# Kernel tuning notes

Measured on AMD Instinct MI355X. Metric: run time of the kernel, lower is better.

## Reference

```python
import jax, jax.numpy as jnp
from jax import lax
import numpy as np

H, W = 240, 304
IN_CH, OUT_CH, K = 16, 32, 3
B = 8
N_PER = 65536
N = B * N_PER
CIN = IN_CH + 2  # pos + neg + features


def setup_inputs() -> dict:
    key = jax.random.key(0)
    k1, k2, k3, k4, k5 = jax.random.split(key, 5)
    # events columns: x, y, t in [0,1); polarity in {0,1}
    xyt = jax.random.uniform(k1, (N, 3), dtype=jnp.float32)
    pol = jax.random.randint(k2, (N, 1), 0, 2).astype(jnp.float32)
    events = jnp.concatenate([xyt, pol], axis=1)
    features = jax.random.normal(k3, (N, IN_CH), dtype=jnp.float32)
    offsets = (jnp.arange(1, B + 1, dtype=jnp.int64) * N_PER)  # cumulative counts
    # SubmanifoldConvolution params: one [CIN, OUT_CH] matrix per filter offset -> HWIO
    fan_in = K * K * CIN
    weight = jax.random.normal(k4, (K, K, CIN, OUT_CH), dtype=jnp.float32) / np.sqrt(fan_in)
    bias = jax.random.normal(k5, (OUT_CH,), dtype=jnp.float32) * 0.01
    return {"events": events, "features": features, "weight": weight,
            "bias": bias, "offsets": offsets}


def reference(events, features, weight, bias, offsets):
    n = events.shape[0]
    b = offsets.shape[0]
    # offset2batch: row i belongs to first sample whose cumulative offset exceeds i
    batch = jnp.searchsorted(offsets, jnp.arange(n, dtype=offsets.dtype), side="right").astype(jnp.int32)
    pos = events[:, 3:4]
    neg = 1.0 - pos
    sparse = jnp.concatenate([pos, neg, features], axis=1)  # [N, CIN]
    # yx = events[:, [1, 0]] scaled by (h, w), rounded to grid coords
    yi = jnp.clip(jnp.round(events[:, 1] * H).astype(jnp.int32), 0, H - 1)
    xi = jnp.clip(jnp.round(events[:, 0] * W).astype(jnp.int32), 0, W - 1)
    key = (batch * H + yi) * W + xi  # linear site id, [N]
    nseg = b * H * W
    # scn InputLayer mode=4: average features of duplicate coordinates
    feat_sum = jax.ops.segment_sum(sparse, key, num_segments=nseg)  # [nseg, CIN]
    cnt = jax.ops.segment_sum(jnp.ones((n,), sparse.dtype), key, num_segments=nseg)
    dense = feat_sum / jnp.maximum(cnt, 1.0)[:, None]
    dense = dense.reshape(b, H, W, CIN)  # zeros at inactive sites
    # Submanifold 3x3 conv: inactive neighbors are zero, so a dense SAME conv
    # evaluated only at active sites matches the submanifold rulebook math.
    out = lax.conv_general_dilated(dense, weight, window_strides=(1, 1),
                                   padding="SAME",
                                   dimension_numbers=("NHWC", "HWIO", "NHWC"))
    out = out.reshape(nseg, OUT_CH)
    # OutputLayer: read back per input row (active sites only), add bias there
    f = out[key] + bias  # [N, OUT_CH]
    return f
```

## Files before the change

kernel.cpp:

```cpp
#include <hip/hip_runtime.h>

#define Hh 240
#define Ww 304
#define IN_CH 16
#define OUT_CH 32
#define Bb 8
#define N_PER 65536
#define N_EV (Bb * N_PER)
#define CIN (IN_CH + 2)
#define NSEG (Bb * Hh * Ww)
#define NBLK 570

#define DP 10

#define TW 32
#define TH 8
#define HW_ 34
#define HH_ 10
#define NXT_TILES 10
#define NYT_TILES 30
#define OPITCH 33
#define HALO_DW (HH_ * HW_ * DP)
#define HALO_LD 3424

typedef __attribute__((ext_vector_type(8))) short bf16x8;
typedef __attribute__((ext_vector_type(4))) float f32x4;

__device__ __forceinline__ unsigned short f2bf(float x) {
  unsigned u = __float_as_uint(x);
  unsigned r = u + 0x7fffu + ((u >> 16) & 1u);
  return (unsigned short)(r >> 16);
}
__device__ __forceinline__ float bf2f(unsigned short b) {
  return __uint_as_float(((unsigned)b) << 16);
}
__device__ __forceinline__ unsigned pk2(float a, float b) {
  return (unsigned)f2bf(a) | ((unsigned)f2bf(b) << 16);
}

__global__ __launch_bounds__(256) void hist_rank_kernel(
    const float* __restrict__ events, const int* __restrict__ offsets,
    int* __restrict__ hist, int2* __restrict__ kr) {
  int i = blockIdx.x * blockDim.x + threadIdx.x;
  float4 ev = ((const float4*)events)[i];
  int yi = (int)rintf(ev.y * (float)Hh);
  yi = min(max(yi, 0), Hh - 1);
  int xi = (int)rintf(ev.x * (float)Ww);
  xi = min(max(xi, 0), Ww - 1);
  int b = 0;
#pragma unroll
  for (int j = 0; j < Bb; j++) b += (offsets[j] <= i) ? 1 : 0;
  int key = (b * Hh + yi) * Ww + xi;
  int pol = (ev.w != 0.0f) ? 1 : 0;
  int rank = atomicAdd(&hist[key], 1);
  kr[i] = make_int2(key | (pol << 31), rank);
}

__global__ __launch_bounds__(256) void scan1_kernel(int* __restrict__ data,
                                                    int* __restrict__ blockSum) {
  __shared__ int lds[256];
  int b = blockIdx.x, t = threadIdx.x;
  int idx = b * 1024 + t * 4;
  int4 v = *(const int4*)(data + idx);
  int s0 = v.x, s1 = s0 + v.y, s2 = s1 + v.z, s3 = s2 + v.w;
  lds[t] = s3;
  __syncthreads();
  int val = s3;
  for (int off = 1; off < 256; off <<= 1) {
    int n = (t >= off) ? lds[t - off] : 0;
    __syncthreads();
    val += n;
    lds[t] = val;
    __syncthreads();
  }
  int excl = val - s3;
  int4 o;
  o.x = excl; o.y = excl + s0; o.z = excl + s1; o.w = excl + s2;
  *(int4*)(data + idx) = o;
  if (t == 255) blockSum[b] = val;
}

__global__ __launch_bounds__(1024) void scan2_weights_kernel(
    const int* __restrict__ blockSum, int* __restrict__ blockOffset,
    const float* __restrict__ weight, unsigned short* __restrict__ wprep) {
  int t = threadIdx.x;
  if (blockIdx.x == 1) {
#pragma unroll
    for (int it = 0; it < 6; it++) {
      int idx = it * 1024 + t;
      int ky = idx >> 11;
      int rem = idx & 2047;
      int n = rem >> 6;
      int kl = rem & 63;
      unsigned short v = 0;
      if (kl < 60) {
        int kx = kl / 20, ci = kl - kx * 20;
        if (ci < 18) v = f2bf(weight[((ky * 3 + kx) * CIN + ci) * OUT_CH + n]);
      }
      wprep[idx] = v;
    }
    return;
  }
  __shared__ int lds[1024];
  int v = (t < NBLK) ? blockSum[t] : 0;
  lds[t] = v;
  __syncthreads();
  int val = v;
  for (int off = 1; off < 1024; off <<= 1) {
    int n = (t >= off) ? lds[t - off] : 0;
    __syncthreads();
    val += n;
    lds[t] = val;
    __syncthreads();
  }
  if (t < NBLK) blockOffset[t] = val - v;
  if (t == 0) blockOffset[NBLK] = lds[1023];
}

__global__ __launch_bounds__(256) void scatter_rec_kernel(
    const float* __restrict__ features, const int2* __restrict__ kr,
    const int* __restrict__ baseLocal, const int* __restrict__ blockOffset,
    uint4* __restrict__ sortedRec, int* __restrict__ sortedMeta) {
  int i = blockIdx.x * blockDim.x + threadIdx.x;
  int2 m = kr[i];
  int key = m.x & 0x7fffffff;
  int pos = baseLocal[key] + blockOffset[key >> 10] + m.y;
  float pol = (float)(((unsigned)m.x) >> 31);
  const float4* f = (const float4*)(features + (size_t)i * IN_CH);
  float4 f0 = f[0], f1 = f[1], f2 = f[2], f3 = f[3];
  uint4* R = sortedRec + (size_t)pos * 4;
  R[0] = make_uint4(pk2(pol, 1.0f - pol), pk2(f0.x, f0.y), pk2(f0.z, f0.w),
                    pk2(f1.x, f1.y));
  R[1] = make_uint4(pk2(f1.z, f1.w), pk2(f2.x, f2.y), pk2(f2.z, f2.w),
                    pk2(f3.x, f3.y));
  R[2] = make_uint4(pk2(f3.z, f3.w), 0, 0, 0);
  R[3] = make_uint4(0, 0, 0, 0);
  int x = key % Ww;
  sortedMeta[pos] = i | (x << 19);
}

__global__ __launch_bounds__(256) void densify_kernel(
    const uint4* __restrict__ sortedRec, const int* __restrict__ baseLocal,
    const int* __restrict__ blockOffset, unsigned* __restrict__ dense) {
  int p = blockIdx.x * 256 + threadIdx.x;
  int bo = blockOffset[p >> 10];
  int base = baseLocal[p] + bo;
  int nxt = ((p & 1023) != 1023) ? (baseLocal[p + 1] + bo)
                                 : blockOffset[(p >> 10) + 1];
  int c = nxt - base;
  float acc[CIN];
#pragma unroll
  for (int k = 0; k < CIN; k++) acc[k] = 0.0f;
  for (int j = 0; j < c; j++) {
    const uint4* R = sortedRec + (size_t)(base + j) * 4;
    uint4 r0 = R[0], r1 = R[1];
    unsigned d8 = ((const unsigned*)R)[8];
    acc[0]  += bf2f((unsigned short)r0.x);  acc[1]  += bf2f((unsigned short)(r0.x >> 16));
    acc[2]  += bf2f((unsigned short)r0.y);  acc[3]  += bf2f((unsigned short)(r0.y >> 16));
    acc[4]  += bf2f((unsigned short)r0.z);  acc[5]  += bf2f((unsigned short)(r0.z >> 16));
    acc[6]  += bf2f((unsigned short)r0.w);  acc[7]  += bf2f((unsigned short)(r0.w >> 16));
    acc[8]  += bf2f((unsigned short)r1.x);  acc[9]  += bf2f((unsigned short)(r1.x >> 16));
    acc[10] += bf2f((unsigned short)r1.y);  acc[11] += bf2f((unsigned short)(r1.y >> 16));
    acc[12] += bf2f((unsigned short)r1.z);  acc[13] += bf2f((unsigned short)(r1.z >> 16));
    acc[14] += bf2f((unsigned short)r1.w);  acc[15] += bf2f((unsigned short)(r1.w >> 16));
    acc[16] += bf2f((unsigned short)d8);    acc[17] += bf2f((unsigned short)(d8 >> 16));
  }
  float inv = 1.0f / fmaxf((float)c, 1.0f);
  unsigned* dp = dense + (size_t)p * DP;
#pragma unroll
  for (int k = 0; k < 9; k++) dp[k] = pk2(acc[2 * k] * inv, acc[2 * k + 1] * inv);
  dp[9] = 0;
}

__global__ __launch_bounds__(256) void fused_conv_kernel(
    const unsigned* __restrict__ dense, const int* __restrict__ sortedMeta,
    const int* __restrict__ baseLocal, const int* __restrict__ blockOffset,
    const unsigned short* __restrict__ wprep, const float* __restrict__ bias,
    float* __restrict__ out) {
  __shared__ unsigned smem[128 * OPITCH];
  __shared__ int rowRg[TH][2];

  int blk = blockIdx.x;
  int xt = blk % NXT_TILES;
  int rem = blk / NXT_TILES;
  int yt = rem % NYT_TILES;
  int b = rem / NYT_TILES;
  int x0 = xt * TW, y0 = yt * TH;
  int tid = threadIdx.x;

  int tx = tid & 31, ty = tid >> 5;
  int gxo = x0 + tx;
  int xlast = min(x0 + TW - 1, Ww - 1);
  if (gxo < Ww) {
    int p = (b * Hh + y0 + ty) * Ww + gxo;
    int bo = blockOffset[p >> 10];
    int base = baseLocal[p] + bo;
    if (tx == 0) rowRg[ty][0] = base;
    if (gxo == xlast) {
      int nxt = ((p & 1023) != 1023) ? (baseLocal[p + 1] + bo)
                                     : blockOffset[(p >> 10) + 1];
      rowRg[ty][1] = nxt;
    }
  }

  for (int i = tid; i < HALO_LD; i += 256) {
    int r = i / 340;
    int cd = i - r * 340;
    int hx = cd / 10;
    int k = cd - hx * 10;
    int gy = y0 - 1 + r, gx = x0 - 1 + hx;
    unsigned v = 0;
    if (gy >= 0 && gy < Hh && gx >= 0 && gx < Ww)
      v = dense[(size_t)((b * Hh + gy) * Ww + gx) * DP + k];
    smem[i] = v;
  }
  __syncthreads();

  int wv = tid >> 6, lane = tid & 63;
  int quad = lane >> 4, lrow = lane & 15;

  f32x4 accf[4][2];
#pragma unroll
  for (int i = 0; i < 4; i++)
#pragma unroll
    for (int nt = 0; nt < 2; nt++) accf[i][nt] = (f32x4){0.f, 0.f, 0.f, 0.f};

  const unsigned* hp = smem;
#pragma unroll
  for (int ky = 0; ky < 3; ky++) {
    bf16x8 bfr[2][2];
#pragma unroll
    for (int kh = 0; kh < 2; kh++)
#pragma unroll
      for (int nt = 0; nt < 2; nt++) {
        int n = nt * 16 + lrow;
        bfr[kh][nt] = *(const bf16x8*)(wprep + ((ky * 32 + n) << 6) +
                                       kh * 32 + quad * 8);
      }
#pragma unroll
    for (int i = 0; i < 4; i++) {
      int t0 = (wv * 4 + i) * 16;
      int ox = (t0 & 31) + lrow;
      int oy = t0 >> 5;
      int pix = (oy + ky) * HW_ + ox;
#pragma unroll
      for (int kh = 0; kh < 2; kh++) {
        union { bf16x8 v; unsigned u[4]; } a;
        int ui = pix * DP + kh * 16 + quad * 4;
        a.u[0] = hp[ui]; a.u[1] = hp[ui + 1];
        a.u[2] = hp[ui + 2]; a.u[3] = hp[ui + 3];
        accf[i][0] = __builtin_amdgcn_mfma_f32_16x16x32_bf16(
            a.v, bfr[kh][0], accf[i][0], 0, 0, 0);
        accf[i][1] = __builtin_amdgcn_mfma_f32_16x16x32_bf16(
            a.v, bfr[kh][1], accf[i][1], 0, 0, 0);
      }
    }
  }
  __syncthreads();

  float* outsh = (float*)smem;
  float bn0 = bias[lrow], bn1 = bias[16 + lrow];
#pragma unroll
  for (int ch = 0; ch < 2; ch++) {
#pragma unroll
    for (int ii = 0; ii < 2; ii++) {
      int i = ch * 2 + ii;
      int lidx = ii * 16 + quad * 4;
      int row = wv * 32 + lidx;
#pragma unroll
      for (int r = 0; r < 4; r++) {
        outsh[(row + r) * OPITCH + lrow] = accf[i][0][r] + bn0;
        outsh[(row + r) * OPITCH + 16 + lrow] = accf[i][1][r] + bn1;
      }
    }
    __syncthreads();
    int lq = tid & 7;
    int grp = tid >> 3;
#pragma unroll
    for (int rr = 0; rr < 4; rr++) {
      int ty2 = ch + rr * 2;
      int rS = rowRg[ty2][0], rE = rowRg[ty2][1];
      for (int s = grp; s < rE - rS; s += 32) {
        unsigned meta = (unsigned)sortedMeta[rS + s];
        int ev = meta & 0x7FFFF;
        int lx = (int)((meta >> 19) & 0x1FF) - x0;
        int pid = ty2 * 32 + lx;
        int orow = ((pid >> 6) << 5) + (((pid >> 4) & 1) << 4) + (pid & 15);
        const float* rp = outsh + orow * OPITCH + (lq << 2);
        float4 v = make_float4(rp[0], rp[1], rp[2], rp[3]);
        ((float4*)(out + (size_t)ev * OUT_CH))[lq] = v;
      }
    }
    __syncthreads();
  }
}

extern "C" void kernel_launch(void* const* d_in, const int* in_sizes, int n_in,
                              void* d_out, int out_size, void* d_ws,
                              size_t ws_size, hipStream_t stream) {
  const float* events = (const float*)d_in[0];
  const float* features = (const float*)d_in[1];
  const float* weight = (const float*)d_in[2];
  const float* bias = (const float*)d_in[3];
  const int* offsets = (const int*)d_in[4];
  float* out = (float*)d_out;

  uint4* sortedRec = (uint4*)d_ws;
  unsigned* dense = (unsigned*)(sortedRec + (size_t)N_EV * 4);
  int* sortedMeta = (int*)(dense + (size_t)NSEG * DP);
  int2* kr = (int2*)(sortedMeta + N_EV);
  int* hist = (int*)(kr + N_EV);
  int* blockOffset = hist + NSEG;
  int* blockSum = blockOffset + 1024;
  unsigned short* wprep = (unsigned short*)(blockSum + 1024);

  hipMemsetAsync(hist, 0, (size_t)NSEG * sizeof(int), stream);

  hist_rank_kernel<<<N_EV / 256, 256, 0, stream>>>(events, offsets, hist, kr);
  scan1_kernel<<<NBLK, 256, 0, stream>>>(hist, blockSum);
  scan2_weights_kernel<<<2, 1024, 0, stream>>>(blockSum, blockOffset, weight,
                                               wprep);
  scatter_rec_kernel<<<N_EV / 256, 256, 0, stream>>>(
      features, kr, hist, blockOffset, sortedRec, sortedMeta);
  densify_kernel<<<NSEG / 256, 256, 0, stream>>>(sortedRec, hist, blockOffset,
                                                 dense);
  fused_conv_kernel<<<Bb * NYT_TILES * NXT_TILES, 256, 0, stream>>>(
      dense, sortedMeta, hist, blockOffset, wprep, bias, out);
}
```

Baseline: 201.5 us.

## Fuse densify into conv halo load and shrink sorted feature records

Removes the separate densify kernel and the dense grid buffer. Each conv block now averages the events of its halo pixels directly from the sorted feature records in shared memory, using a tightly packed 18-channel layout that matches a reworked weight prep. The sorted records shrink to 32 bytes of features, and polarity moves into a spare bit of the metadata word. In exchange, halo pixels are re-averaged by every neighbouring tile, and the gather loop over events runs with variable trip count inside the conv kernel, adding divergence.

```diff
diff --git a/kernel.cpp b/kernel.cpp
--- a/kernel.cpp
+++ b/kernel.cpp
@@ -11,17 +11,14 @@
 #define NSEG (Bb * Hh * Ww)
 #define NBLK 570
 
-#define DP 10
-
 #define TW 32
 #define TH 8
 #define HW_ 34
 #define HH_ 10
+#define HALO_PIX (HH_ * HW_)
 #define NXT_TILES 10
 #define NYT_TILES 30
 #define OPITCH 33
-#define HALO_DW (HH_ * HW_ * DP)
-#define HALO_LD 3424
 
 typedef __attribute__((ext_vector_type(8))) short bf16x8;
 typedef __attribute__((ext_vector_type(4))) float f32x4;
@@ -93,9 +90,9 @@
       int n = rem >> 6;
       int kl = rem & 63;
       unsigned short v = 0;
-      if (kl < 60) {
-        int kx = kl / 20, ci = kl - kx * 20;
-        if (ci < 18) v = f2bf(weight[((ky * 3 + kx) * CIN + ci) * OUT_CH + n]);
+      if (kl < 54) {
+        int kx = kl / 18, ci = kl - kx * 18;
+        v = f2bf(weight[((ky * 3 + kx) * CIN + ci) * OUT_CH + n]);
       }
       wprep[idx] = v;
     }
@@ -117,63 +114,29 @@
   if (t == 0) blockOffset[NBLK] = lds[1023];
 }
 
-__global__ __launch_bounds__(256) void scatter_rec_kernel(
+__global__ __launch_bounds__(256) void scatter_feat_kernel(
     const float* __restrict__ features, const int2* __restrict__ kr,
     const int* __restrict__ baseLocal, const int* __restrict__ blockOffset,
-    uint4* __restrict__ sortedRec, int* __restrict__ sortedMeta) {
+    uint4* __restrict__ sortedFeat, int* __restrict__ sortedMeta) {
   int i = blockIdx.x * blockDim.x + threadIdx.x;
   int2 m = kr[i];
   int key = m.x & 0x7fffffff;
   int pos = baseLocal[key] + blockOffset[key >> 10] + m.y;
-  float pol = (float)(((unsigned)m.x) >> 31);
   const float4* f = (const float4*)(features + (size_t)i * IN_CH);
   float4 f0 = f[0], f1 = f[1], f2 = f[2], f3 = f[3];
-  uint4* R = sortedRec + (size_t)pos * 4;
-  R[0] = make_uint4(pk2(pol, 1.0f - pol), pk2(f0.x, f0.y), pk2(f0.z, f0.w),
-                    pk2(f1.x, f1.y));
-  R[1] = make_uint4(pk2(f1.z, f1.w), pk2(f2.x, f2.y), pk2(f2.z, f2.w),
-                    pk2(f3.x, f3.y));
-  R[2] = make_uint4(pk2(f3.z, f3.w), 0, 0, 0);
-  R[3] = make_uint4(0, 0, 0, 0);
+  uint4 w0, w1;
+  w0.x = pk2(f0.x, f0.y); w0.y = pk2(f0.z, f0.w);
+  w0.z = pk2(f1.x, f1.y); w0.w = pk2(f1.z, f1.w);
+  w1.x = pk2(f2.x, f2.y); w1.y = pk2(f2.z, f2.w);
+  w1.z = pk2(f3.x, f3.y); w1.w = pk2(f3.z, f3.w);
+  sortedFeat[(size_t)pos * 2] = w0;
+  sortedFeat[(size_t)pos * 2 + 1] = w1;
   int x = key % Ww;
-  sortedMeta[pos] = i | (x << 19);
-}
-
-__global__ __launch_bounds__(256) void densify_kernel(
-    const uint4* __restrict__ sortedRec, const int* __restrict__ baseLocal,
-    const int* __restrict__ blockOffset, unsigned* __restrict__ dense) {
-  int p = blockIdx.x * 256 + threadIdx.x;
-  int bo = blockOffset[p >> 10];
-  int base = baseLocal[p] + bo;
-  int nxt = ((p & 1023) != 1023) ? (baseLocal[p + 1] + bo)
-                                 : blockOffset[(p >> 10) + 1];
-  int c = nxt - base;
-  float acc[CIN];
-#pragma unroll
-  for (int k = 0; k < CIN; k++) acc[k] = 0.0f;
-  for (int j = 0; j < c; j++) {
-    const uint4* R = sortedRec + (size_t)(base + j) * 4;
-    uint4 r0 = R[0], r1 = R[1];
-    unsigned d8 = ((const unsigned*)R)[8];
-    acc[0]  += bf2f((unsigned short)r0.x);  acc[1]  += bf2f((unsigned short)(r0.x >> 16));
-    acc[2]  += bf2f((unsigned short)r0.y);  acc[3]  += bf2f((unsigned short)(r0.y >> 16));
-    acc[4]  += bf2f((unsigned short)r0.z);  acc[5]  += bf2f((unsigned short)(r0.z >> 16));
-    acc[6]  += bf2f((unsigned short)r0.w);  acc[7]  += bf2f((unsigned short)(r0.w >> 16));
-    acc[8]  += bf2f((unsigned short)r1.x);  acc[9]  += bf2f((unsigned short)(r1.x >> 16));
-    acc[10] += bf2f((unsigned short)r1.y);  acc[11] += bf2f((unsigned short)(r1.y >> 16));
-    acc[12] += bf2f((unsigned short)r1.z);  acc[13] += bf2f((unsigned short)(r1.z >> 16));
-    acc[14] += bf2f((unsigned short)r1.w);  acc[15] += bf2f((unsigned short)(r1.w >> 16));
-    acc[16] += bf2f((unsigned short)d8);    acc[17] += bf2f((unsigned short)(d8 >> 16));
-  }
-  float inv = 1.0f / fmaxf((float)c, 1.0f);
-  unsigned* dp = dense + (size_t)p * DP;
-#pragma unroll
-  for (int k = 0; k < 9; k++) dp[k] = pk2(acc[2 * k] * inv, acc[2 * k + 1] * inv);
-  dp[9] = 0;
+  sortedMeta[pos] = i | (x << 19) | (m.x & (int)0x80000000);
 }
 
 __global__ __launch_bounds__(256) void fused_conv_kernel(
-    const unsigned* __restrict__ dense, const int* __restrict__ sortedMeta,
+    const uint4* __restrict__ sortedFeat, const int* __restrict__ sortedMeta,
     const int* __restrict__ baseLocal, const int* __restrict__ blockOffset,
     const unsigned short* __restrict__ wprep, const float* __restrict__ bias,
     float* __restrict__ out) {
@@ -187,6 +150,8 @@
   int b = rem / NYT_TILES;
   int x0 = xt * TW, y0 = yt * TH;
   int tid = threadIdx.x;
+
+  if (tid < 12) smem[3060 + tid] = 0;
 
   int tx = tid & 31, ty = tid >> 5;
   int gxo = x0 + tx;
@@ -203,16 +168,42 @@
     }
   }
 
-  for (int i = tid; i < HALO_LD; i += 256) {
-    int r = i / 340;
-    int cd = i - r * 340;
-    int hx = cd / 10;
-    int k = cd - hx * 10;
-    int gy = y0 - 1 + r, gx = x0 - 1 + hx;
-    unsigned v = 0;
-    if (gy >= 0 && gy < Hh && gx >= 0 && gx < Ww)
-      v = dense[(size_t)((b * Hh + gy) * Ww + gx) * DP + k];
-    smem[i] = v;
+  for (int h = tid; h < HALO_PIX; h += 256) {
+    int hy = h / HW_, hx = h % HW_;
+    int gy = y0 - 1 + hy, gx = x0 - 1 + hx;
+    float acc[CIN];
+#pragma unroll
+    for (int k = 0; k < CIN; k++) acc[k] = 0.0f;
+    int c = 0, base = 0;
+    if (gy >= 0 && gy < Hh && gx >= 0 && gx < Ww) {
+      int p = (b * Hh + gy) * Ww + gx;
+      int bo = blockOffset[p >> 10];
+      base = baseLocal[p] + bo;
+      int nxt = ((p & 1023) != 1023) ? (baseLocal[p + 1] + bo)
+                                     : blockOffset[(p >> 10) + 1];
+      c = nxt - base;
+      for (int j = 0; j < c; j++) {
+        int e = sortedMeta[base + j];
+        float pol = (float)((unsigned)e >> 31);
+        acc[0] += pol;
+        acc[1] += 1.0f - pol;
+        uint4 w0 = sortedFeat[(size_t)(base + j) * 2];
+        uint4 w1 = sortedFeat[(size_t)(base + j) * 2 + 1];
+        acc[2] += bf2f((unsigned short)w0.x);  acc[3] += bf2f((unsigned short)(w0.x >> 16));
+        acc[4] += bf2f((unsigned short)w0.y);  acc[5] += bf2f((unsigned short)(w0.y >> 16));
+        acc[6] += bf2f((unsigned short)w0.z);  acc[7] += bf2f((unsigned short)(w0.z >> 16));
+        acc[8] += bf2f((unsigned short)w0.w);  acc[9] += bf2f((unsigned short)(w0.w >> 16));
+        acc[10] += bf2f((unsigned short)w1.x); acc[11] += bf2f((unsigned short)(w1.x >> 16));
+        acc[12] += bf2f((unsigned short)w1.y); acc[13] += bf2f((unsigned short)(w1.y >> 16));
+        acc[14] += bf2f((unsigned short)w1.z); acc[15] += bf2f((unsigned short)(w1.z >> 16));
+        acc[16] += bf2f((unsigned short)w1.w); acc[17] += bf2f((unsigned short)(w1.w >> 16));
+      }
+    }
+    float inv = 1.0f / fmaxf((float)c, 1.0f);
+    unsigned* row = smem + 9 * h;
+#pragma unroll
+    for (int k = 0; k < 9; k++)
+      row[k] = pk2(acc[2 * k] * inv, acc[2 * k + 1] * inv);
   }
   __syncthreads();
 
@@ -242,11 +233,11 @@
       int t0 = (wv * 4 + i) * 16;
       int ox = (t0 & 31) + lrow;
       int oy = t0 >> 5;
-      int pix = (oy + ky) * HW_ + ox;
+      int idx0 = ((oy + ky) * HW_ + ox) * CIN;
 #pragma unroll
       for (int kh = 0; kh < 2; kh++) {
         union { bf16x8 v; unsigned u[4]; } a;
-        int ui = pix * DP + kh * 16 + quad * 4;
+        int ui = (idx0 >> 1) + kh * 16 + quad * 4;
         a.u[0] = hp[ui]; a.u[1] = hp[ui + 1];
         a.u[2] = hp[ui + 2]; a.u[3] = hp[ui + 3];
         accf[i][0] = __builtin_amdgcn_mfma_f32_16x16x32_bf16(
@@ -305,9 +296,8 @@
   const int* offsets = (const int*)d_in[4];
   float* out = (float*)d_out;
 
-  uint4* sortedRec = (uint4*)d_ws;
-  unsigned* dense = (unsigned*)(sortedRec + (size_t)N_EV * 4);
-  int* sortedMeta = (int*)(dense + (size_t)NSEG * DP);
+  uint4* sortedFeat = (uint4*)d_ws;
+  int* sortedMeta = (int*)(sortedFeat + (size_t)N_EV * 2);
   int2* kr = (int2*)(sortedMeta + N_EV);
   int* hist = (int*)(kr + N_EV);
   int* blockOffset = hist + NSEG;
@@ -320,10 +310,8 @@
   scan1_kernel<<<NBLK, 256, 0, stream>>>(hist, blockSum);
   scan2_weights_kernel<<<2, 1024, 0, stream>>>(blockSum, blockOffset, weight,
                                                wprep);
-  scatter_rec_kernel<<<N_EV / 256, 256, 0, stream>>>(
-      features, kr, hist, blockOffset, sortedRec, sortedMeta);
-  densify_kernel<<<NSEG / 256, 256, 0, stream>>>(sortedRec, hist, blockOffset,
-                                                 dense);
+  scatter_feat_kernel<<<N_EV / 256, 256, 0, stream>>>(
+      features, kr, hist, blockOffset, sortedFeat, sortedMeta);
   fused_conv_kernel<<<Bb * NYT_TILES * NXT_TILES, 256, 0, stream>>>(
-      dense, sortedMeta, hist, blockOffset, wprep, bias, out);
-}
+      sortedFeat, sortedMeta, hist, blockOffset, wprep, bias, out);
+}
```

After: 181.1 us. 10.1% less time.
